# Kernel optimization log

Measured on AMD Instinct MI355X. Metric: run time of the kernel, lower is better.

The kernel has to match this reference:

```python
import jax, jax.numpy as jnp
import numpy as np

B, H, SQ, SKV, D = 2, 16, 2048, 3072, 64
NUM_PT = 1024  # SKV = NUM_PT + SQ


def setup_inputs() -> dict:
    key = jax.random.key(0)
    kq, kk, kv = jax.random.split(key, 3)
    q = jax.random.normal(kq, (B, H, SQ, D), dtype=jnp.float32)
    k = jax.random.normal(kk, (B, H, SKV, D), dtype=jnp.float32)
    v = jax.random.normal(kv, (B, H, SKV, D), dtype=jnp.float32)
    return {"q": q, "k": k, "v": v, "num_pt": NUM_PT}


def _prefix_causal_mask(sq, skv, num_pt):
    # kv_idx < num_pt always visible (global prefix); otherwise causal on
    # shifted index: q_idx >= kv_idx - num_pt
    q_idx = jnp.arange(sq)[:, None]   # [SQ,1]
    kv_idx = jnp.arange(skv)[None, :]  # [1,SKV]
    return (kv_idx < num_pt) | (q_idx >= kv_idx - num_pt)  # [SQ,SKV]


def reference(q, k, v, num_pt):
    scale = 1.0 / jnp.sqrt(jnp.asarray(q.shape[-1], q.dtype))
    # [B,H,SQ,SKV]
    scores = jnp.einsum("bhqd,bhkd->bhqk", q, k) * scale
    mask = _prefix_causal_mask(q.shape[2], k.shape[2], num_pt)  # [SQ,SKV]
    neg = jnp.asarray(jnp.finfo(scores.dtype).min, scores.dtype)
    scores = jnp.where(mask[None, None], scores, neg)
    probs = jax.nn.softmax(scores, axis=-1)
    return jnp.einsum("bhqk,bhkd->bhqd", probs, v)
```

## Files before the change

kernel.cpp:

```cpp
#include <hip/hip_runtime.h>

#define B_ 2
#define H_ 16
#define SQ_ 2048
#define SKV_ 3072
#define DH 64
#define QT 128
#define KVT 64
#define LDK 72

typedef __attribute__((ext_vector_type(4))) float f32x4;
typedef __attribute__((ext_vector_type(8))) short bf16x8;

__device__ __forceinline__ unsigned pk2(float a, float b) {
  return __builtin_amdgcn_perm(__float_as_uint(b) + 0x8000u,
                               __float_as_uint(a) + 0x8000u, 0x07060302u);
}
__device__ __forceinline__ short bf1(float a) {
  return (short)((__float_as_uint(a) + 0x8000u) >> 16);
}

__global__ __launch_bounds__(512, 4) void attn_fwd(
    const float* __restrict__ qg_, const float* __restrict__ kg_,
    const float* __restrict__ vg_, const int* __restrict__ num_pt_p,
    float* __restrict__ og_) {
  __shared__ __align__(16) short Ks[KVT][LDK];
  __shared__ __align__(16) short Vt[DH][LDK];
  __shared__ __align__(16) short Ps[8][16][LDK];

  const int tid  = (int)threadIdx.x;
  const int lane = tid & 63;
  const int w    = tid >> 6;
  const int lq   = lane & 15;
  const int quad = lane >> 4;
  const int qb   = (SQ_ / QT) - 1 - (int)blockIdx.x;
  const int bh   = (int)blockIdx.y;
  const int num_pt = *num_pt_p;
  const int q0   = qb * QT;

  const float* qg = qg_ + (size_t)bh * SQ_ * DH;
  const float* kg = kg_ + (size_t)bh * SKV_ * DH;
  const float* vg = vg_ + (size_t)bh * SKV_ * DH;
  float*       og = og_ + (size_t)bh * SQ_ * DH;

  const float SC = 0.125f * 1.44269504088896341f;

  const int qrow = q0 + w * 16 + lq;
  bf16x8 qf[2];
  {
    const float* qp = qg + (size_t)qrow * DH + quad * 8;
#pragma unroll
    for (int kh = 0; kh < 2; ++kh) {
      float4 a = *(const float4*)(qp + kh * 32);
      float4 b = *(const float4*)(qp + kh * 32 + 4);
      union { unsigned u[4]; bf16x8 h; } t;
      t.u[0] = pk2(a.x * SC, a.y * SC);
      t.u[1] = pk2(a.z * SC, a.w * SC);
      t.u[2] = pk2(b.x * SC, b.y * SC);
      t.u[3] = pk2(b.z * SC, b.w * SC);
      qf[kh] = t.h;
    }
  }

  f32x4 O[4];
#pragma unroll
  for (int i = 0; i < 4; ++i) O[i] = (f32x4){0.f, 0.f, 0.f, 0.f};
  float m_run = -__builtin_inff();
  float l_run = 0.f;

  int n_tiles = (q0 + QT - 1 + num_pt) / KVT + 1;
  if (n_tiles > SKV_ / KVT) n_tiles = SKV_ / KVT;

  const int krow = tid >> 3;
  const int kcol = (tid & 7) * 8;
  const int vkv  = tid & 63;
  const int vd0  = (tid >> 6) * 8;
  const float* kQp = kg + (size_t)krow * DH + kcol;
  const float* vQp = vg + (size_t)vkv * DH + vd0;

  float4 kf[2], vf[2];
  kf[0] = *(const float4*)(kQp);
  kf[1] = *(const float4*)(kQp + 4);
  vf[0] = *(const float4*)(vQp);
  vf[1] = *(const float4*)(vQp + 4);

  const int lim = qrow + num_pt;

  for (int t = 0; t < n_tiles; ++t) {
    const int kb = t * KVT;
    __syncthreads();

    {
      union { unsigned u[4]; bf16x8 h; } tk;
      tk.u[0] = pk2(kf[0].x, kf[0].y);
      tk.u[1] = pk2(kf[0].z, kf[0].w);
      tk.u[2] = pk2(kf[1].x, kf[1].y);
      tk.u[3] = pk2(kf[1].z, kf[1].w);
      *(bf16x8*)&Ks[krow][kcol] = tk.h;
      Vt[vd0 + 0][vkv] = bf1(vf[0].x);
      Vt[vd0 + 1][vkv] = bf1(vf[0].y);
      Vt[vd0 + 2][vkv] = bf1(vf[0].z);
      Vt[vd0 + 3][vkv] = bf1(vf[0].w);
      Vt[vd0 + 4][vkv] = bf1(vf[1].x);
      Vt[vd0 + 5][vkv] = bf1(vf[1].y);
      Vt[vd0 + 6][vkv] = bf1(vf[1].z);
      Vt[vd0 + 7][vkv] = bf1(vf[1].w);
    }
    if (t + 1 < n_tiles) {
      const size_t nb = (size_t)(kb + KVT) * DH;
      kf[0] = *(const float4*)(kQp + nb);
      kf[1] = *(const float4*)(kQp + nb + 4);
      vf[0] = *(const float4*)(vQp + nb);
      vf[1] = *(const float4*)(vQp + nb + 4);
    }
    __syncthreads();

    f32x4 st[4];
#pragma unroll
    for (int mg = 0; mg < 4; ++mg) {
      bf16x8 ka0 = *(const bf16x8*)&Ks[mg * 16 + lq][quad * 8];
      bf16x8 ka1 = *(const bf16x8*)&Ks[mg * 16 + lq][32 + quad * 8];
      f32x4 c = (f32x4){0.f, 0.f, 0.f, 0.f};
      c = __builtin_amdgcn_mfma_f32_16x16x32_bf16(ka0, qf[0], c, 0, 0, 0);
      c = __builtin_amdgcn_mfma_f32_16x16x32_bf16(ka1, qf[1], c, 0, 0, 0);
      st[mg] = c;
    }

    if (kb + KVT - 1 > q0 + w * 16 + num_pt) {
#pragma unroll
      for (int mg = 0; mg < 4; ++mg)
#pragma unroll
        for (int r = 0; r < 4; ++r)
          if (kb + mg * 16 + quad * 4 + r > lim) st[mg][r] = -__builtin_inff();
    }

    float mx = st[0][0];
#pragma unroll
    for (int mg = 0; mg < 4; ++mg)
#pragma unroll
      for (int r = 0; r < 4; ++r) mx = fmaxf(mx, st[mg][r]);
    mx = fmaxf(mx, __shfl_xor(mx, 16));
    mx = fmaxf(mx, __shfl_xor(mx, 32));
    float m_new = fmaxf(m_run, mx);
    float ts = 0.f;
#pragma unroll
    for (int mg = 0; mg < 4; ++mg)
#pragma unroll
      for (int r = 0; r < 4; ++r) {
        float pe = __builtin_amdgcn_exp2f(st[mg][r] - m_new);
        st[mg][r] = pe;
        ts += pe;
      }
    if (__any(m_new > m_run)) {
      float alpha = __builtin_amdgcn_exp2f(m_run - m_new);
      l_run = l_run * alpha + ts;
      m_run = m_new;
#pragma unroll
      for (int dg = 0; dg < 4; ++dg)
#pragma unroll
        for (int r = 0; r < 4; ++r) O[dg][r] *= alpha;
    } else {
      l_run += ts;
    }

#pragma unroll
    for (int mg = 0; mg < 4; ++mg) {
      *(uint2*)&Ps[w][lq][mg * 16 + quad * 4] =
          make_uint2(pk2(st[mg][0], st[mg][1]), pk2(st[mg][2], st[mg][3]));
    }
    bf16x8 pa0 = *(const bf16x8*)&Ps[w][lq][quad * 8];
    bf16x8 pa1 = *(const bf16x8*)&Ps[w][lq][32 + quad * 8];
#pragma unroll
    for (int dg = 0; dg < 4; ++dg) {
      bf16x8 vb0 = *(const bf16x8*)&Vt[dg * 16 + lq][quad * 8];
      bf16x8 vb1 = *(const bf16x8*)&Vt[dg * 16 + lq][32 + quad * 8];
      O[dg] = __builtin_amdgcn_mfma_f32_16x16x32_bf16(vb0, pa0, O[dg], 0, 0, 0);
      O[dg] = __builtin_amdgcn_mfma_f32_16x16x32_bf16(vb1, pa1, O[dg], 0, 0, 0);
    }
  }

  l_run += __shfl_xor(l_run, 16);
  l_run += __shfl_xor(l_run, 32);
  float inv = 1.0f / l_run;
  float* op = og + (size_t)qrow * DH + quad * 4;
#pragma unroll
  for (int dg = 0; dg < 4; ++dg) {
    float4 o4;
    o4.x = O[dg][0] * inv;
    o4.y = O[dg][1] * inv;
    o4.z = O[dg][2] * inv;
    o4.w = O[dg][3] * inv;
    *(float4*)(op + dg * 16) = o4;
  }
}

extern "C" void kernel_launch(void* const* d_in, const int* in_sizes, int n_in,
                              void* d_out, int out_size, void* d_ws, size_t ws_size,
                              hipStream_t stream) {
  const float* q = (const float*)d_in[0];
  const float* k = (const float*)d_in[1];
  const float* v = (const float*)d_in[2];
  const int* np  = (const int*)d_in[3];
  float* out = (float*)d_out;
  dim3 grid(SQ_ / QT, B_ * H_);
  attn_fwd<<<grid, dim3(512), 0, stream>>>(q, k, v, np, out);
}
```

Before: 187.5 us.

## Split each KV window across two wave groups and merge softmax partials

Blocks grow to 1024 threads. The two halves of the 16 waves each process one 64-row half of a 128-row KV window, keeping separate running max, sum and output, which are combined through shared memory at the end. V staging now packs two kv rows into one 32-bit LDS store, and the query-block order is reversed for only half of the batch-head index to spread causal work more evenly. The goal is more waves in flight and fewer loop iterations per block. The cost is a larger LDS footprint, an extra merge step, and more wasted masked work in the final window.

```diff
diff --git a/kernel.cpp b/kernel.cpp
--- a/kernel.cpp
+++ b/kernel.cpp
@@ -6,7 +6,7 @@
 #define SKV_ 3072
 #define DH 64
 #define QT 128
-#define KVT 64
+#define WKV 128
 #define LDK 72
 
 typedef __attribute__((ext_vector_type(4))) float f32x4;
@@ -16,25 +16,27 @@
   return __builtin_amdgcn_perm(__float_as_uint(b) + 0x8000u,
                                __float_as_uint(a) + 0x8000u, 0x07060302u);
 }
-__device__ __forceinline__ short bf1(float a) {
-  return (short)((__float_as_uint(a) + 0x8000u) >> 16);
-}
-
-__global__ __launch_bounds__(512, 4) void attn_fwd(
+
+__global__ __launch_bounds__(1024, 8) void attn_fwd(
     const float* __restrict__ qg_, const float* __restrict__ kg_,
     const float* __restrict__ vg_, const int* __restrict__ num_pt_p,
     float* __restrict__ og_) {
-  __shared__ __align__(16) short Ks[KVT][LDK];
-  __shared__ __align__(16) short Vt[DH][LDK];
-  __shared__ __align__(16) short Ps[8][16][LDK];
+  __shared__ __align__(16) short Ks[WKV][LDK];
+  __shared__ __align__(16) short Vt[2][DH][LDK];
+  __shared__ __align__(16) short Ps[16][16][LDK];
+  __shared__ float Ml[8][64][2];
 
   const int tid  = (int)threadIdx.x;
   const int lane = tid & 63;
   const int w    = tid >> 6;
+  const int qw   = w & 7;
+  const int h    = w >> 3;
   const int lq   = lane & 15;
   const int quad = lane >> 4;
-  const int qb   = (SQ_ / QT) - 1 - (int)blockIdx.x;
-  const int bh   = (int)blockIdx.y;
+  const int x    = (int)blockIdx.x;
+  const int y    = (int)blockIdx.y;
+  const int qb   = (y & 16) ? x : (15 - x);
+  const int bh   = y;
   const int num_pt = *num_pt_p;
   const int q0   = qb * QT;
 
@@ -45,7 +47,7 @@
 
   const float SC = 0.125f * 1.44269504088896341f;
 
-  const int qrow = q0 + w * 16 + lq;
+  const int qrow = q0 + qw * 16 + lq;
   bf16x8 qf[2];
   {
     const float* qp = qg + (size_t)qrow * DH + quad * 8;
@@ -53,12 +55,12 @@
     for (int kh = 0; kh < 2; ++kh) {
       float4 a = *(const float4*)(qp + kh * 32);
       float4 b = *(const float4*)(qp + kh * 32 + 4);
-      union { unsigned u[4]; bf16x8 h; } t;
+      union { unsigned u[4]; bf16x8 hh; } t;
       t.u[0] = pk2(a.x * SC, a.y * SC);
       t.u[1] = pk2(a.z * SC, a.w * SC);
       t.u[2] = pk2(b.x * SC, b.y * SC);
       t.u[3] = pk2(b.z * SC, b.w * SC);
-      qf[kh] = t.h;
+      qf[kh] = t.hh;
     }
   }
 
@@ -68,65 +70,62 @@
   float m_run = -__builtin_inff();
   float l_run = 0.f;
 
-  int n_tiles = (q0 + QT - 1 + num_pt) / KVT + 1;
-  if (n_tiles > SKV_ / KVT) n_tiles = SKV_ / KVT;
+  int n_win = (q0 + QT - 1 + num_pt) / WKV + 1;
+  if (n_win > SKV_ / WKV) n_win = SKV_ / WKV;
 
   const int krow = tid >> 3;
   const int kcol = (tid & 7) * 8;
-  const int vkv  = tid & 63;
-  const int vd0  = (tid >> 6) * 8;
+  const int vp   = tid & 63;
+  const int vh   = vp >> 5;
+  const int vkv  = (2 * vp) & 63;
+  const int vd0  = (tid >> 6) * 4;
   const float* kQp = kg + (size_t)krow * DH + kcol;
-  const float* vQp = vg + (size_t)vkv * DH + vd0;
-
-  float4 kf[2], vf[2];
-  kf[0] = *(const float4*)(kQp);
-  kf[1] = *(const float4*)(kQp + 4);
-  vf[0] = *(const float4*)(vQp);
-  vf[1] = *(const float4*)(vQp + 4);
+  const float* vQp = vg + (size_t)(2 * vp) * DH + vd0;
+
+  float4 kf0 = *(const float4*)(kQp);
+  float4 kf1 = *(const float4*)(kQp + 4);
+  float4 vfa = *(const float4*)(vQp);
+  float4 vfb = *(const float4*)(vQp + DH);
 
   const int lim = qrow + num_pt;
 
-  for (int t = 0; t < n_tiles; ++t) {
-    const int kb = t * KVT;
+  for (int t = 0; t < n_win; ++t) {
+    const int kb = t * WKV + h * 64;
     __syncthreads();
 
     {
-      union { unsigned u[4]; bf16x8 h; } tk;
-      tk.u[0] = pk2(kf[0].x, kf[0].y);
-      tk.u[1] = pk2(kf[0].z, kf[0].w);
-      tk.u[2] = pk2(kf[1].x, kf[1].y);
-      tk.u[3] = pk2(kf[1].z, kf[1].w);
-      *(bf16x8*)&Ks[krow][kcol] = tk.h;
-      Vt[vd0 + 0][vkv] = bf1(vf[0].x);
-      Vt[vd0 + 1][vkv] = bf1(vf[0].y);
-      Vt[vd0 + 2][vkv] = bf1(vf[0].z);
-      Vt[vd0 + 3][vkv] = bf1(vf[0].w);
-      Vt[vd0 + 4][vkv] = bf1(vf[1].x);
-      Vt[vd0 + 5][vkv] = bf1(vf[1].y);
-      Vt[vd0 + 6][vkv] = bf1(vf[1].z);
-      Vt[vd0 + 7][vkv] = bf1(vf[1].w);
-    }
-    if (t + 1 < n_tiles) {
-      const size_t nb = (size_t)(kb + KVT) * DH;
-      kf[0] = *(const float4*)(kQp + nb);
-      kf[1] = *(const float4*)(kQp + nb + 4);
-      vf[0] = *(const float4*)(vQp + nb);
-      vf[1] = *(const float4*)(vQp + nb + 4);
+      union { unsigned u[4]; bf16x8 hh; } tk;
+      tk.u[0] = pk2(kf0.x, kf0.y);
+      tk.u[1] = pk2(kf0.z, kf0.w);
+      tk.u[2] = pk2(kf1.x, kf1.y);
+      tk.u[3] = pk2(kf1.z, kf1.w);
+      *(bf16x8*)&Ks[krow][kcol] = tk.hh;
+      *(unsigned*)&Vt[vh][vd0 + 0][vkv] = pk2(vfa.x, vfb.x);
+      *(unsigned*)&Vt[vh][vd0 + 1][vkv] = pk2(vfa.y, vfb.y);
+      *(unsigned*)&Vt[vh][vd0 + 2][vkv] = pk2(vfa.z, vfb.z);
+      *(unsigned*)&Vt[vh][vd0 + 3][vkv] = pk2(vfa.w, vfb.w);
+    }
+    if (t + 1 < n_win) {
+      const size_t nb = (size_t)(t + 1) * WKV * DH;
+      kf0 = *(const float4*)(kQp + nb);
+      kf1 = *(const float4*)(kQp + nb + 4);
+      vfa = *(const float4*)(vQp + nb);
+      vfb = *(const float4*)(vQp + nb + DH);
     }
     __syncthreads();
 
     f32x4 st[4];
 #pragma unroll
     for (int mg = 0; mg < 4; ++mg) {
-      bf16x8 ka0 = *(const bf16x8*)&Ks[mg * 16 + lq][quad * 8];
-      bf16x8 ka1 = *(const bf16x8*)&Ks[mg * 16 + lq][32 + quad * 8];
+      bf16x8 ka0 = *(const bf16x8*)&Ks[h * 64 + mg * 16 + lq][quad * 8];
+      bf16x8 ka1 = *(const bf16x8*)&Ks[h * 64 + mg * 16 + lq][32 + quad * 8];
       f32x4 c = (f32x4){0.f, 0.f, 0.f, 0.f};
       c = __builtin_amdgcn_mfma_f32_16x16x32_bf16(ka0, qf[0], c, 0, 0, 0);
       c = __builtin_amdgcn_mfma_f32_16x16x32_bf16(ka1, qf[1], c, 0, 0, 0);
       st[mg] = c;
     }
 
-    if (kb + KVT - 1 > q0 + w * 16 + num_pt) {
+    if (kb + 63 > q0 + qw * 16 + num_pt) {
 #pragma unroll
       for (int mg = 0; mg < 4; ++mg)
 #pragma unroll
@@ -172,8 +171,8 @@
     bf16x8 pa1 = *(const bf16x8*)&Ps[w][lq][32 + quad * 8];
 #pragma unroll
     for (int dg = 0; dg < 4; ++dg) {
-      bf16x8 vb0 = *(const bf16x8*)&Vt[dg * 16 + lq][quad * 8];
-      bf16x8 vb1 = *(const bf16x8*)&Vt[dg * 16 + lq][32 + quad * 8];
+      bf16x8 vb0 = *(const bf16x8*)&Vt[h][dg * 16 + lq][quad * 8];
+      bf16x8 vb1 = *(const bf16x8*)&Vt[h][dg * 16 + lq][32 + quad * 8];
       O[dg] = __builtin_amdgcn_mfma_f32_16x16x32_bf16(vb0, pa0, O[dg], 0, 0, 0);
       O[dg] = __builtin_amdgcn_mfma_f32_16x16x32_bf16(vb1, pa1, O[dg], 0, 0, 0);
     }
@@ -181,16 +180,35 @@
 
   l_run += __shfl_xor(l_run, 16);
   l_run += __shfl_xor(l_run, 32);
-  float inv = 1.0f / l_run;
-  float* op = og + (size_t)qrow * DH + quad * 4;
-#pragma unroll
-  for (int dg = 0; dg < 4; ++dg) {
-    float4 o4;
-    o4.x = O[dg][0] * inv;
-    o4.y = O[dg][1] * inv;
-    o4.z = O[dg][2] * inv;
-    o4.w = O[dg][3] * inv;
-    *(float4*)(op + dg * 16) = o4;
+
+  float* Ov = (float*)&Ps[0][0][0];
+  __syncthreads();
+  if (h == 1) {
+    Ml[qw][lane][0] = m_run;
+    Ml[qw][lane][1] = l_run;
+#pragma unroll
+    for (int dg = 0; dg < 4; ++dg)
+      *(f32x4*)&Ov[(((qw * 4 + dg) * 64) + lane) * 4] = O[dg];
+  }
+  __syncthreads();
+  if (h == 0) {
+    float m1 = Ml[qw][lane][0];
+    float l1 = Ml[qw][lane][1];
+    float M  = fmaxf(m_run, m1);
+    float a0 = __builtin_amdgcn_exp2f(m_run - M);
+    float a1 = __builtin_amdgcn_exp2f(m1 - M);
+    float inv = 1.0f / (l_run * a0 + l1 * a1);
+    float* op = og + (size_t)qrow * DH + quad * 4;
+#pragma unroll
+    for (int dg = 0; dg < 4; ++dg) {
+      f32x4 o1 = *(const f32x4*)&Ov[(((qw * 4 + dg) * 64) + lane) * 4];
+      float4 o4;
+      o4.x = (O[dg][0] * a0 + o1[0] * a1) * inv;
+      o4.y = (O[dg][1] * a0 + o1[1] * a1) * inv;
+      o4.z = (O[dg][2] * a0 + o1[2] * a1) * inv;
+      o4.w = (O[dg][3] * a0 + o1[3] * a1) * inv;
+      *(float4*)(op + dg * 16) = o4;
+    }
   }
 }
 
@@ -203,5 +221,5 @@
   const int* np  = (const int*)d_in[3];
   float* out = (float*)d_out;
   dim3 grid(SQ_ / QT, B_ * H_);
-  attn_fwd<<<grid, dim3(512), 0, stream>>>(q, k, v, np, out);
+  attn_fwd<<<grid, dim3(1024), 0, stream>>>(q, k, v, np, out);
 }
```

Measured after the change: 373.6 us. +99.3%, slower.

## Double-buffer K/V shared tiles, pack V transpose stores, interleave causal block order

Applied to the files above, without the earlier changes.

Adds a second shared-memory buffer for K and V so the next tile is stored after the PV MFMAs. This leaves one barrier per iteration instead of two. The V transpose store now packs two kv rows into one 32-bit LDS write, replacing eight 16-bit writes per thread. Block order alternates between ascending and descending query tiles depending on blockIdx.y bit 4, to balance causal work across the grid. The cost is extra LDS per block, which could reduce occupancy.

```diff
diff --git a/kernel.cpp b/kernel.cpp
--- a/kernel.cpp
+++ b/kernel.cpp
@@ -16,16 +16,13 @@
   return __builtin_amdgcn_perm(__float_as_uint(b) + 0x8000u,
                                __float_as_uint(a) + 0x8000u, 0x07060302u);
 }
-__device__ __forceinline__ short bf1(float a) {
-  return (short)((__float_as_uint(a) + 0x8000u) >> 16);
-}
 
 __global__ __launch_bounds__(512, 4) void attn_fwd(
     const float* __restrict__ qg_, const float* __restrict__ kg_,
     const float* __restrict__ vg_, const int* __restrict__ num_pt_p,
     float* __restrict__ og_) {
-  __shared__ __align__(16) short Ks[KVT][LDK];
-  __shared__ __align__(16) short Vt[DH][LDK];
+  __shared__ __align__(16) short Ks[2][KVT][LDK];
+  __shared__ __align__(16) short Vt[2][DH][LDK];
   __shared__ __align__(16) short Ps[8][16][LDK];
 
   const int tid  = (int)threadIdx.x;
@@ -33,15 +30,16 @@
   const int w    = tid >> 6;
   const int lq   = lane & 15;
   const int quad = lane >> 4;
-  const int qb   = (SQ_ / QT) - 1 - (int)blockIdx.x;
-  const int bh   = (int)blockIdx.y;
+  const int x    = (int)blockIdx.x;
+  const int y    = (int)blockIdx.y;
+  const int qb   = (y & 16) ? x : (15 - x);
   const int num_pt = *num_pt_p;
   const int q0   = qb * QT;
 
-  const float* qg = qg_ + (size_t)bh * SQ_ * DH;
-  const float* kg = kg_ + (size_t)bh * SKV_ * DH;
-  const float* vg = vg_ + (size_t)bh * SKV_ * DH;
-  float*       og = og_ + (size_t)bh * SQ_ * DH;
+  const float* qg = qg_ + (size_t)y * SQ_ * DH;
+  const float* kg = kg_ + (size_t)y * SKV_ * DH;
+  const float* vg = vg_ + (size_t)y * SKV_ * DH;
+  float*       og = og_ + (size_t)y * SQ_ * DH;
 
   const float SC = 0.125f * 1.44269504088896341f;
 
@@ -53,12 +51,12 @@
     for (int kh = 0; kh < 2; ++kh) {
       float4 a = *(const float4*)(qp + kh * 32);
       float4 b = *(const float4*)(qp + kh * 32 + 4);
-      union { unsigned u[4]; bf16x8 h; } t;
+      union { unsigned u[4]; bf16x8 hh; } t;
       t.u[0] = pk2(a.x * SC, a.y * SC);
       t.u[1] = pk2(a.z * SC, a.w * SC);
       t.u[2] = pk2(b.x * SC, b.y * SC);
       t.u[3] = pk2(b.z * SC, b.w * SC);
-      qf[kh] = t.h;
+      qf[kh] = t.hh;
     }
   }
 
@@ -73,53 +71,50 @@
 
   const int krow = tid >> 3;
   const int kcol = (tid & 7) * 8;
-  const int vkv  = tid & 63;
-  const int vd0  = (tid >> 6) * 8;
+  const int vp   = tid & 31;
+  const int vd0  = (tid >> 5) * 4;
   const float* kQp = kg + (size_t)krow * DH + kcol;
-  const float* vQp = vg + (size_t)vkv * DH + vd0;
-
-  float4 kf[2], vf[2];
-  kf[0] = *(const float4*)(kQp);
-  kf[1] = *(const float4*)(kQp + 4);
-  vf[0] = *(const float4*)(vQp);
-  vf[1] = *(const float4*)(vQp + 4);
+  const float* vQp = vg + (size_t)(2 * vp) * DH + vd0;
+
+  float4 kf0 = *(const float4*)(kQp);
+  float4 kf1 = *(const float4*)(kQp + 4);
+  float4 vfa = *(const float4*)(vQp);
+  float4 vfb = *(const float4*)(vQp + DH);
+
+  {
+    union { unsigned u[4]; bf16x8 hh; } tk;
+    tk.u[0] = pk2(kf0.x, kf0.y);
+    tk.u[1] = pk2(kf0.z, kf0.w);
+    tk.u[2] = pk2(kf1.x, kf1.y);
+    tk.u[3] = pk2(kf1.z, kf1.w);
+    *(bf16x8*)&Ks[0][krow][kcol] = tk.hh;
+    *(unsigned*)&Vt[0][vd0 + 0][2 * vp] = pk2(vfa.x, vfb.x);
+    *(unsigned*)&Vt[0][vd0 + 1][2 * vp] = pk2(vfa.y, vfb.y);
+    *(unsigned*)&Vt[0][vd0 + 2][2 * vp] = pk2(vfa.z, vfb.z);
+    *(unsigned*)&Vt[0][vd0 + 3][2 * vp] = pk2(vfa.w, vfb.w);
+  }
+  __syncthreads();
 
   const int lim = qrow + num_pt;
 
   for (int t = 0; t < n_tiles; ++t) {
     const int kb = t * KVT;
-    __syncthreads();
-
-    {
-      union { unsigned u[4]; bf16x8 h; } tk;
-      tk.u[0] = pk2(kf[0].x, kf[0].y);
-      tk.u[1] = pk2(kf[0].z, kf[0].w);
-      tk.u[2] = pk2(kf[1].x, kf[1].y);
-      tk.u[3] = pk2(kf[1].z, kf[1].w);
-      *(bf16x8*)&Ks[krow][kcol] = tk.h;
-      Vt[vd0 + 0][vkv] = bf1(vf[0].x);
-      Vt[vd0 + 1][vkv] = bf1(vf[0].y);
-      Vt[vd0 + 2][vkv] = bf1(vf[0].z);
-      Vt[vd0 + 3][vkv] = bf1(vf[0].w);
-      Vt[vd0 + 4][vkv] = bf1(vf[1].x);
-      Vt[vd0 + 5][vkv] = bf1(vf[1].y);
-      Vt[vd0 + 6][vkv] = bf1(vf[1].z);
-      Vt[vd0 + 7][vkv] = bf1(vf[1].w);
-    }
-    if (t + 1 < n_tiles) {
-      const size_t nb = (size_t)(kb + KVT) * DH;
-      kf[0] = *(const float4*)(kQp + nb);
-      kf[1] = *(const float4*)(kQp + nb + 4);
-      vf[0] = *(const float4*)(vQp + nb);
-      vf[1] = *(const float4*)(vQp + nb + 4);
-    }
-    __syncthreads();
+    const int buf = t & 1;
+    const bool more = (t + 1 < n_tiles);
+
+    if (more) {
+      const size_t nb = (size_t)(t + 1) * KVT * DH;
+      kf0 = *(const float4*)(kQp + nb);
+      kf1 = *(const float4*)(kQp + nb + 4);
+      vfa = *(const float4*)(vQp + nb);
+      vfb = *(const float4*)(vQp + nb + DH);
+    }
 
     f32x4 st[4];
 #pragma unroll
     for (int mg = 0; mg < 4; ++mg) {
-      bf16x8 ka0 = *(const bf16x8*)&Ks[mg * 16 + lq][quad * 8];
-      bf16x8 ka1 = *(const bf16x8*)&Ks[mg * 16 + lq][32 + quad * 8];
+      bf16x8 ka0 = *(const bf16x8*)&Ks[buf][mg * 16 + lq][quad * 8];
+      bf16x8 ka1 = *(const bf16x8*)&Ks[buf][mg * 16 + lq][32 + quad * 8];
       f32x4 c = (f32x4){0.f, 0.f, 0.f, 0.f};
       c = __builtin_amdgcn_mfma_f32_16x16x32_bf16(ka0, qf[0], c, 0, 0, 0);
       c = __builtin_amdgcn_mfma_f32_16x16x32_bf16(ka1, qf[1], c, 0, 0, 0);
@@ -172,11 +167,25 @@
     bf16x8 pa1 = *(const bf16x8*)&Ps[w][lq][32 + quad * 8];
 #pragma unroll
     for (int dg = 0; dg < 4; ++dg) {
-      bf16x8 vb0 = *(const bf16x8*)&Vt[dg * 16 + lq][quad * 8];
-      bf16x8 vb1 = *(const bf16x8*)&Vt[dg * 16 + lq][32 + quad * 8];
+      bf16x8 vb0 = *(const bf16x8*)&Vt[buf][dg * 16 + lq][quad * 8];
+      bf16x8 vb1 = *(const bf16x8*)&Vt[buf][dg * 16 + lq][32 + quad * 8];
       O[dg] = __builtin_amdgcn_mfma_f32_16x16x32_bf16(vb0, pa0, O[dg], 0, 0, 0);
       O[dg] = __builtin_amdgcn_mfma_f32_16x16x32_bf16(vb1, pa1, O[dg], 0, 0, 0);
     }
+
+    if (more) {
+      union { unsigned u[4]; bf16x8 hh; } tk;
+      tk.u[0] = pk2(kf0.x, kf0.y);
+      tk.u[1] = pk2(kf0.z, kf0.w);
+      tk.u[2] = pk2(kf1.x, kf1.y);
+      tk.u[3] = pk2(kf1.z, kf1.w);
+      *(bf16x8*)&Ks[buf ^ 1][krow][kcol] = tk.hh;
+      *(unsigned*)&Vt[buf ^ 1][vd0 + 0][2 * vp] = pk2(vfa.x, vfb.x);
+      *(unsigned*)&Vt[buf ^ 1][vd0 + 1][2 * vp] = pk2(vfa.y, vfb.y);
+      *(unsigned*)&Vt[buf ^ 1][vd0 + 2][2 * vp] = pk2(vfa.z, vfb.z);
+      *(unsigned*)&Vt[buf ^ 1][vd0 + 3][2 * vp] = pk2(vfa.w, vfb.w);
+    }
+    __syncthreads();
   }
 
   l_run += __shfl_xor(l_run, 16);
```

Result: faster. 166.8 us (-11.0%).
